# Kernel optimization log

Hardware: AMD Instinct MI355X
Metric: run time of the kernel (lower is better)

Reference implementation:

```python
import jax, jax.numpy as jnp
import numpy as np
from jax import lax

B, CIN, COUT, K, SDIM, H = 8, 512, 512, 3, 512, 32
EPS = 1e-8
LRELU_SLOPE = 0.2
ACT_SCALE = float(np.sqrt(2.0))


def setup_inputs() -> dict:
    key = jax.random.key(0)
    k1, k2, k3, k4 = jax.random.split(key, 4)
    return {
        "x": jax.random.normal(k1, (B, CIN, H, H), jnp.float32),
        "style": jax.random.normal(k2, (B, SDIM), jnp.float32),
        "weight": jax.random.normal(k3, (COUT, CIN, K, K), jnp.float32),
        "mod_w": jax.random.normal(k4, (CIN, SDIM), jnp.float32),
        "mod_b": jnp.ones((CIN,), jnp.float32),  # EqualLinear bias_init=1
        "bias": jnp.zeros((COUT,), jnp.float32),  # FusedLeakyReLU bias
    }


def _blur_kernel(c):
    bk = np.array([1.0, 3.0, 3.0, 1.0], np.float32)
    bk = bk[None, :] * bk[:, None]
    bk = bk / bk.sum() * 4.0  # upsample_factor ** 2
    return jnp.tile(jnp.asarray(bk)[None, None], (c, 1, 1, 1))  # (C,1,4,4)


def reference(x, style, weight, mod_w, mod_b, bias):
    b, cin, h, w = x.shape
    cout, k = weight.shape[0], weight.shape[-1]
    conv_scale = 1.0 / np.sqrt(cin * k * k)
    lin_scale = 1.0 / np.sqrt(mod_w.shape[1])

    # style modulation: EqualLinear(style_dim -> in_channel), bias_init=1
    s = style @ (mod_w * lin_scale).T + mod_b  # (B, Cin)

    # per-sample modulated weights (B, Cout, Cin, k, k)
    wmod = conv_scale * weight[None] * s[:, None, :, None, None]
    demod = lax.rsqrt(jnp.sum(wmod * wmod, axis=(2, 3, 4)) + EPS)
    wmod = wmod * demod[:, :, None, None, None]

    # conv_transpose2d(stride=2, pad=0) == conv with lhs_dilation=2, pad=k-1,
    # spatially-flipped kernel (torch transposes (Cout,Cin)->(Cin,Cout)).
    wflip = jnp.flip(wmod, (-2, -1))

    def convt(xi, wi):  # xi: (Cin,H,W), wi: (Cout,Cin,k,k)
        return lax.conv_general_dilated(
            xi[None], wi, (1, 1), [(k - 1, k - 1)] * 2,
            lhs_dilation=(2, 2),
            dimension_numbers=("NCHW", "OIHW", "NCHW"))[0]

    y = jax.vmap(convt)(x, wflip)  # (B, Cout, 2H+1, 2W+1)

    # Blur: upfirdn2d with pad=(1,1), depthwise 4x4 FIR (kernel symmetric)
    bk = _blur_kernel(cout)
    y = lax.conv_general_dilated(
        y, bk, (1, 1), [(1, 1), (1, 1)],
        feature_group_count=cout,
        dimension_numbers=("NCHW", "OIHW", "NCHW"))  # (B, Cout, 2H, 2W)

    # FusedLeakyReLU: leaky_relu(y + bias) * sqrt(2)
    z = y + bias[None, :, None, None]
    return jnp.where(z >= 0, z, LRELU_SLOPE * z) * ACT_SCALE
```

## Files before the change

### kernel.cpp

```cpp
#include <hip/hip_runtime.h>
#include <hip/hip_bf16.h>

#define NB 8
#define CIN 512
#define COUT 512
#define SDIM 512

typedef __attribute__((ext_vector_type(8))) short short8;
typedef __attribute__((ext_vector_type(4))) float f32x4;

static constexpr float CONV_SCALE = 0.014731391274719740f;
static constexpr float LIN_SCALE  = 0.044194173824159216f;

static constexpr size_t OFF_S     = 0;
static constexpr size_t OFF_WSQ   = 16384;
static constexpr size_t OFF_DEMOD = 1064960;
static constexpr size_t OFF_XP    = 1081344;
static constexpr size_t OFF_WP    = 10551296;
static constexpr size_t OFF_Y1    = 15269888;

static constexpr int NJOBS = 1060;

__device__ __forceinline__ int wpoff(int ps) {
  return ps == 0 ? 0 : ps == 1 ? 1048576 : ps == 2 ? 1572864 : 2097152;
}
__device__ __forceinline__ constexpr int PSPAD(int ps) {
  return ps == 0 ? 1090 : ps == 3 ? 1024 : 1056;
}
__device__ __forceinline__ constexpr int PLB(int ps) {
  return ps == 0 ? 0 : ps == 1 ? 4464640 : ps == 2 ? 8790016 : 13115392;
}

__device__ __forceinline__ short f2bf(float f) {
  unsigned u = __builtin_bit_cast(unsigned, f);
  unsigned r = (u + 0x7fffu + ((u >> 16) & 1u)) >> 16;
  return (short)r;
}
__device__ __forceinline__ float bf2f(unsigned short u) {
  return __builtin_bit_cast(float, (unsigned)u << 16);
}

__device__ __forceinline__ void load_lds16(const short* g, short* l) {
  __builtin_amdgcn_global_load_lds(
      (const __attribute__((address_space(1))) unsigned int*)g,
      (__attribute__((address_space(3))) unsigned int*)l, 16, 0, 0);
}

__global__ void k_prep1(const float* __restrict__ style, const float* __restrict__ mod_w,
                        const float* __restrict__ mod_b, float* __restrict__ s_out,
                        const float* __restrict__ w, short* __restrict__ wp,
                        float* __restrict__ wsq) {
  const int tid = threadIdx.x;
  if (blockIdx.x < 1024) {
    int idx = blockIdx.x * 256 + tid;
    int co = idx >> 9, ci = idx & 511;
    float wv[3][3];
    float sq = 0.f;
#pragma unroll
    for (int i = 0; i < 9; ++i) {
      float v = w[idx * 9 + i];
      wv[i / 3][i % 3] = v;
      sq += v * v;
    }
    wsq[idx] = sq * CONV_SCALE * CONV_SCALE;
#pragma unroll
    for (int wy = 0; wy < 3; ++wy)
#pragma unroll
      for (int wx = 0; wx < 3; ++wx) {
        int psy = (wy == 1) ? 1 : 0, psx = (wx == 1) ? 1 : 0;
        int u = psy ? 0 : (wy == 0 ? 1 : 0);
        int v = psx ? 0 : (wx == 0 ? 1 : 0);
        int ps = psy * 2 + psx;
        int tap = psy ? (psx ? 0 : v) : (psx ? u : u * 2 + v);
        int k = tap * 512 + ci;
        int elem = wpoff(ps) + ((k >> 6) * 512 + co) * 64 + (k & 63);
        wp[elem] = f2bf(wv[wy][wx] * CONV_SCALE);
      }
  } else {
    int wid = tid >> 6, lane = tid & 63;
    int ci = (blockIdx.x - 1024) * 4 + wid;
    float acc[NB] = {};
    for (int k = lane; k < SDIM; k += 64) {
      float wm = mod_w[ci * SDIM + k];
#pragma unroll
      for (int b = 0; b < NB; ++b) acc[b] += wm * style[b * SDIM + k];
    }
#pragma unroll
    for (int b = 0; b < NB; ++b) {
      float v = acc[b];
      for (int o = 32; o > 0; o >>= 1) v += __shfl_xor(v, o);
      if (lane == 0) s_out[b * CIN + ci] = v * LIN_SCALE + mod_b[ci];
    }
  }
}

__global__ void k_prep2(const float* __restrict__ wsq, const float* __restrict__ s,
                        float* __restrict__ demod,
                        const float* __restrict__ x, short* __restrict__ xp) {
  const int tid = threadIdx.x;
  if (blockIdx.x < 1024) {
    __shared__ float t[64][65];
    const int tx = tid & 63, ty = tid >> 6;
    int bx = blockIdx.x;
    int sp0 = (bx & 15) * 64, ci0 = ((bx >> 4) & 7) * 64, b = bx >> 7;
    for (int r = ty; r < 64; r += 4)
      t[r][tx] = x[(b * CIN + ci0 + r) * 1024 + sp0 + tx];
    __syncthreads();
    int ci = ci0 + tx;
    float sv = s[b * CIN + ci];
    for (int r = ty; r < 64; r += 4) {
      int sp = sp0 + r;
      int yy = sp >> 5, xx = sp & 31;
      xp[((b * 34 + yy + 1) * 34 + (xx + 1)) * 512 + ci] = f2bf(t[tx][r] * sv);
    }
  } else if (blockIdx.x < 1152) {
    int wid = tid >> 6, lane = tid & 63;
    int co = (blockIdx.x - 1024) * 4 + wid;
    float acc[NB] = {};
    for (int ci = lane; ci < CIN; ci += 64) {
      float wq = wsq[co * CIN + ci];
#pragma unroll
      for (int b = 0; b < NB; ++b) {
        float sv = s[b * CIN + ci];
        acc[b] += wq * sv * sv;
      }
    }
#pragma unroll
    for (int b = 0; b < NB; ++b) {
      float v = acc[b];
      for (int o = 32; o > 0; o >>= 1) v += __shfl_xor(v, o);
      if (lane == 0) demod[b * COUT + co] = rsqrtf(v + 1e-8f);
    }
  } else {
    int idx = blockIdx.x - 1152;
    int b = idx >> 2, part = idx & 3;
    unsigned* xpu = (unsigned*)xp;
    for (int k = 0; k < 33; ++k) {
      int c = part * 33 + k;
      int yy, xx;
      if (c < 34)       { yy = 0;            xx = c; }
      else if (c < 68)  { yy = 33;           xx = c - 34; }
      else if (c < 100) { yy = 1 + (c - 68); xx = 0; }
      else              { yy = 1 + (c - 100); xx = 33; }
      xpu[((((b * 34 + yy) * 34 + xx) * 512) >> 1) + tid] = 0u;
    }
  }
}

__global__ __launch_bounds__(256, 4) void k_gemm(const short* __restrict__ xp,
                                                 const short* __restrict__ wp,
                                                 short* __restrict__ y1) {
  __shared__ short sW[2][128 * 32];
  __shared__ short sX[2][128 * 32];

  const int tid = threadIdx.x;
  const int wid = tid >> 6, lane = tid & 63;
  const int hi = lane >> 4;
  const int wm = (wid >> 1) * 64, wn = (wid & 1) * 64;

  const int bx = blockIdx.x;
  const int xcd = bx & 7, ii = bx >> 3;
  const int j = (((ii >> 2) << 3) + xcd) * 4 + (ii & 3);
  if (j >= NJOBS) return;

  int ps, base;
  if (j < 276)      { ps = 0; base = 0; }
  else if (j < 540) { ps = 1; base = 276; }
  else if (j < 804) { ps = 2; base = 540; }
  else              { ps = 3; base = 804; }
  const int r = j - base;
  const int nb = r >> 2, mb = r & 3;
  const int psy = ps >> 1, psx = ps & 1;
  const int Ny = 33 - psy, Nx = 33 - psx;
  const int NyNx = Ny * Nx;
  const int N = NB * NyNx;
  const int n0 = nb * 128, m0 = mb * 128;
  const int KT32 = (2 - psy) * (2 - psx) * 16;
  const short* wpb = wp + wpoff(ps);

  int bb2[2], ay2[2], ax2[2];
#pragma unroll
  for (int i = 0; i < 2; ++i) {
    int n = n0 + i * 64 + (tid >> 2);
    if (n >= N) n = N - 1;
    int b = n / NyNx;
    int rem = n - b * NyNx;
    int a_y = rem / Nx;
    bb2[i] = b; ay2[i] = a_y; ax2[i] = rem - a_y * Nx;
  }

  auto STAGE = [&](int kt, int d) {
    int tap = kt >> 4, ci0 = (kt & 15) << 5;
    int oy, ox;
    if (ps == 0)      { oy = tap >> 1; ox = tap & 1; }
    else if (ps == 1) { oy = tap;      ox = 1; }
    else if (ps == 2) { oy = 1;        ox = tap; }
    else              { oy = 1;        ox = 1; }
#pragma unroll
    for (int i = 0; i < 2; ++i) {
      int seg = i * 256 + tid;
      int row = seg >> 2;
      int clog = (seg & 3) ^ ((row >> 1) & 3);
      const short* gw = wpb + ((kt >> 1) * 512 + m0 + row) * 64 + (kt & 1) * 32 + clog * 8;
      load_lds16(gw, &sW[d][seg * 8]);
    }
#pragma unroll
    for (int i = 0; i < 2; ++i) {
      int seg = i * 256 + tid;
      int row = seg >> 2;
      int clog = (seg & 3) ^ ((row >> 1) & 3);
      const short* gx = xp + ((bb2[i] * 34 + ay2[i] + oy) * 34 + ax2[i] + ox) * 512 + ci0 + clog * 8;
      load_lds16(gx, &sX[d][seg * 8]);
    }
  };

  int offA[4], offB[4];
#pragma unroll
  for (int f = 0; f < 4; ++f) {
    int ra = wm + f * 16 + (lane & 15);
    offA[f] = ra * 32 + ((hi ^ ((ra >> 1) & 3)) * 8);
    int rb = wn + f * 16 + (lane & 15);
    offB[f] = rb * 32 + ((hi ^ ((rb >> 1) & 3)) * 8);
  }

  f32x4 acc[4][4] = {};

  STAGE(0, 0);
  STAGE(1, 1);
  __syncthreads();

  for (int t = 0; t < KT32; ++t) {
    const short* W = sW[t & 1];
    const short* X = sX[t & 1];
    short8 af[4], bf[4];
#pragma unroll
    for (int f = 0; f < 4; ++f) af[f] = *(const short8*)&W[offA[f]];
#pragma unroll
    for (int f = 0; f < 4; ++f) bf[f] = *(const short8*)&X[offB[f]];

    __builtin_amdgcn_s_setprio(1);
#pragma unroll
    for (int mf = 0; mf < 4; ++mf)
#pragma unroll
      for (int nf = 0; nf < 4; ++nf)
        acc[mf][nf] = __builtin_amdgcn_mfma_f32_16x16x32_bf16(af[mf], bf[nf], acc[mf][nf], 0, 0, 0);
    __builtin_amdgcn_s_setprio(0);

    __syncthreads();
    if (t + 2 < KT32) STAGE(t + 2, t & 1);
  }

  const int psp = PSPAD(ps);
  const int plb = PLB(ps);
#pragma unroll
  for (int nf = 0; nf < 4; ++nf) {
    int n = n0 + wn + nf * 16 + (lane & 15);
    if (n < N) {
      int b = n / NyNx;
      int rem = n - b * NyNx;
      int nbase = plb + b * psp + rem;
#pragma unroll
      for (int mf = 0; mf < 4; ++mf) {
        int m = m0 + wm + mf * 16 + (lane >> 4) * 4;
#pragma unroll
        for (int rr = 0; rr < 4; ++rr)
          y1[nbase + (m + rr) * 8 * psp] = f2bf(acc[mf][nf][rr]);
      }
    }
  }
}

__global__ __launch_bounds__(256, 8) void k_blur(const short* __restrict__ y1,
                                                 const float* __restrict__ demod,
                                                 const float* __restrict__ bias,
                                                 float* __restrict__ out) {
  __shared__ float sin_[4][18 * 35];
  __shared__ float stmp[2][18][64];
  const int tid = threadIdx.x;
  const int bc = blockIdx.x & 4095;
  const int h = blockIdx.x >> 12;
  const int co = bc & 511, b = bc >> 9;
  const int m0v = h * 16;

  for (int i = tid; i < 4 * 18 * 35; i += 256) ((float*)sin_)[i] = 0.f;
  __syncthreads();

#pragma unroll
  for (int ps = 0; ps < 4; ++ps) {
    const int Nyv = 33 - (ps >> 1), Nxv = 33 - (ps & 1);
    const int total = Nyv * Nxv;
    const int estart = (h == 0) ? 0 : (m0v - 1) * Nxv;
    const int es = estart & ~1;
    const int eend = min(total, (m0v + 17) * Nxv);
    const short* pl = y1 + PLB(ps) + (co * NB + b) * PSPAD(ps);
    for (int e0 = es + tid * 2; e0 < eend; e0 += 512) {
      unsigned pair = *(const unsigned*)&pl[e0];
      int av0 = e0 / Nxv, ah0 = e0 - av0 * Nxv;
      int lr0 = av0 + 1 - m0v;
      if (lr0 >= 0 && lr0 < 18)
        sin_[ps][lr0 * 35 + ah0 + 1] = bf2f((unsigned short)(pair & 0xffffu));
      int e1 = e0 + 1;
      if (e1 < total) {
        int av1 = e1 / Nxv, ah1 = e1 - av1 * Nxv;
        int lr1 = av1 + 1 - m0v;
        if (lr1 >= 0 && lr1 < 18)
          sin_[ps][lr1 * 35 + ah1 + 1] = bf2f((unsigned short)(pair >> 16));
      }
    }
  }
  __syncthreads();

  const int q = tid & 63;
  const int mx = q >> 1, fx = q & 1;
  int xp0, xi0, xp1, xi1, xp2, xi2, xp3, xi3;
  if (fx) { xp0 = 0; xi0 = mx + 1; xp1 = 1; xi1 = mx + 1; xp2 = 0; xi2 = mx + 2; xp3 = 1; xi3 = mx + 2; }
  else    { xp0 = 1; xi0 = mx;     xp1 = 0; xi1 = mx + 1; xp2 = 1; xi2 = mx + 1; xp3 = 0; xi3 = mx + 2; }

  for (int rt = tid >> 6; rt < 36; rt += 4) {
    int pv = (rt >= 18) ? 1 : 0;
    int lr = rt - pv * 18;
    if (m0v + lr < 35) {
      float v = 0.25f * sin_[pv * 2 + xp0][lr * 35 + xi0]
              + 0.75f * sin_[pv * 2 + xp1][lr * 35 + xi1]
              + 0.75f * sin_[pv * 2 + xp2][lr * 35 + xi2]
              + 0.25f * sin_[pv * 2 + xp3][lr * 35 + xi3];
      stmp[pv][lr][q] = v;
    } else {
      stmp[pv][lr][q] = 0.f;
    }
  }
  __syncthreads();

  const float dm = demod[b * COUT + co], bs = bias[co];
  for (int pl_ = tid >> 6; pl_ < 32; pl_ += 4) {
    int myl = pl_ >> 1, fy = pl_ & 1;
    float v;
    if (fy) v = 0.25f * stmp[0][myl + 1][q] + 0.75f * stmp[1][myl + 1][q]
              + 0.75f * stmp[0][myl + 2][q] + 0.25f * stmp[1][myl + 2][q];
    else    v = 0.25f * stmp[1][myl][q]     + 0.75f * stmp[0][myl + 1][q]
              + 0.75f * stmp[1][myl + 1][q] + 0.25f * stmp[0][myl + 2][q];
    float val = dm * v + bs;
    int p = h * 32 + pl_;
    out[(bc * 64 + p) * 64 + q] = (val >= 0.f ? val : 0.2f * val) * 1.41421356237309515f;
  }
}

extern "C" void kernel_launch(void* const* d_in, const int* in_sizes, int n_in,
                              void* d_out, int out_size, void* d_ws, size_t ws_size,
                              hipStream_t stream) {
  const float* x      = (const float*)d_in[0];
  const float* style  = (const float*)d_in[1];
  const float* weight = (const float*)d_in[2];
  const float* mod_w  = (const float*)d_in[3];
  const float* mod_b  = (const float*)d_in[4];
  const float* bias   = (const float*)d_in[5];
  float* out = (float*)d_out;
  char* ws = (char*)d_ws;

  float* s     = (float*)(ws + OFF_S);
  float* wsq   = (float*)(ws + OFF_WSQ);
  float* demod = (float*)(ws + OFF_DEMOD);
  short* xp    = (short*)(ws + OFF_XP);
  short* wp    = (short*)(ws + OFF_WP);
  short* y1    = (short*)(ws + OFF_Y1);

  k_prep1<<<1152, 256, 0, stream>>>(style, mod_w, mod_b, s, weight, wp, wsq);
  k_prep2<<<1184, 256, 0, stream>>>(wsq, s, demod, x, xp);
  k_gemm<<<1088, 256, 0, stream>>>(xp, wp, y1);
  k_blur<<<8192, 256, 0, stream>>>(y1, demod, bias, out);
}
```

Baseline: 115.5 us.

## Enlarge GEMM block tile to 128x256 with each wave covering all M rows

The transposed-conv GEMM block tile grows from 128x128 to 128 (M) x 256 (N). Each of the four waves now computes a 128x64 slab instead of a 64x64 quadrant, and job counts and the grid are halved to match. Each X row's base pointer is precomputed and the swizzle offset hoisted out of the staging loop to cut address arithmetic. This roughly halves the number of times weight tiles are loaded per output and raises MFMA work per LDS read. In exchange it doubles accumulator registers and LDS per block, which lowers occupancy (launch bounds drop to 2 blocks per CU) and makes the last wave of blocks coarser.

```diff
diff --git a/kernel.cpp b/kernel.cpp
--- a/kernel.cpp
+++ b/kernel.cpp
@@ -19,7 +19,7 @@
 static constexpr size_t OFF_WP    = 10551296;
 static constexpr size_t OFF_Y1    = 15269888;
 
-static constexpr int NJOBS = 1060;
+static constexpr int NJOBS = 532;
 
 __device__ __forceinline__ int wpoff(int ps) {
   return ps == 0 ? 0 : ps == 1 ? 1048576 : ps == 2 ? 1572864 : 2097152;
@@ -147,16 +147,16 @@
   }
 }
 
-__global__ __launch_bounds__(256, 4) void k_gemm(const short* __restrict__ xp,
+__global__ __launch_bounds__(256, 2) void k_gemm(const short* __restrict__ xp,
                                                  const short* __restrict__ wp,
                                                  short* __restrict__ y1) {
-  __shared__ short sW[2][128 * 32];
-  __shared__ short sX[2][128 * 32];
+  __shared__ short sW[2][4096];
+  __shared__ short sX[2][8192];
 
   const int tid = threadIdx.x;
   const int wid = tid >> 6, lane = tid & 63;
   const int hi = lane >> 4;
-  const int wm = (wid >> 1) * 64, wn = (wid & 1) * 64;
+  const int wn = wid * 64;
 
   const int bx = blockIdx.x;
   const int xcd = bx & 7, ii = bx >> 3;
@@ -164,30 +164,32 @@
   if (j >= NJOBS) return;
 
   int ps, base;
-  if (j < 276)      { ps = 0; base = 0; }
-  else if (j < 540) { ps = 1; base = 276; }
-  else if (j < 804) { ps = 2; base = 540; }
-  else              { ps = 3; base = 804; }
+  if (j < 140)      { ps = 0; base = 0; }
+  else if (j < 272) { ps = 1; base = 140; }
+  else if (j < 404) { ps = 2; base = 272; }
+  else              { ps = 3; base = 404; }
   const int r = j - base;
   const int nb = r >> 2, mb = r & 3;
   const int psy = ps >> 1, psx = ps & 1;
   const int Ny = 33 - psy, Nx = 33 - psx;
   const int NyNx = Ny * Nx;
   const int N = NB * NyNx;
-  const int n0 = nb * 128, m0 = mb * 128;
+  const int n0 = nb * 256, m0 = mb * 128;
   const int KT32 = (2 - psy) * (2 - psx) * 16;
   const short* wpb = wp + wpoff(ps);
 
-  int bb2[2], ay2[2], ax2[2];
-#pragma unroll
-  for (int i = 0; i < 2; ++i) {
+  const short* xbase[4];
+#pragma unroll
+  for (int i = 0; i < 4; ++i) {
     int n = n0 + i * 64 + (tid >> 2);
     if (n >= N) n = N - 1;
     int b = n / NyNx;
     int rem = n - b * NyNx;
     int a_y = rem / Nx;
-    bb2[i] = b; ay2[i] = a_y; ax2[i] = rem - a_y * Nx;
-  }
+    int a_x = rem - a_y * Nx;
+    xbase[i] = xp + ((b * 34 + a_y) * 34 + a_x) * 512;
+  }
+  const int clog8 = (((tid & 3) ^ ((tid >> 3) & 3)) * 8);
 
   auto STAGE = [&](int kt, int d) {
     int tap = kt >> 4, ci0 = (kt & 15) << 5;
@@ -196,34 +198,33 @@
     else if (ps == 1) { oy = tap;      ox = 1; }
     else if (ps == 2) { oy = 1;        ox = tap; }
     else              { oy = 1;        ox = 1; }
+    const int goffX = (oy * 34 + ox) * 512 + ci0 + clog8;
 #pragma unroll
     for (int i = 0; i < 2; ++i) {
       int seg = i * 256 + tid;
-      int row = seg >> 2;
-      int clog = (seg & 3) ^ ((row >> 1) & 3);
-      const short* gw = wpb + ((kt >> 1) * 512 + m0 + row) * 64 + (kt & 1) * 32 + clog * 8;
+      const short* gw = wpb + ((kt >> 1) * 512 + m0 + (seg >> 2)) * 64 + (kt & 1) * 32 + clog8;
       load_lds16(gw, &sW[d][seg * 8]);
     }
 #pragma unroll
-    for (int i = 0; i < 2; ++i) {
+    for (int i = 0; i < 4; ++i) {
       int seg = i * 256 + tid;
-      int row = seg >> 2;
-      int clog = (seg & 3) ^ ((row >> 1) & 3);
-      const short* gx = xp + ((bb2[i] * 34 + ay2[i] + oy) * 34 + ax2[i] + ox) * 512 + ci0 + clog * 8;
-      load_lds16(gx, &sX[d][seg * 8]);
+      load_lds16(xbase[i] + goffX, &sX[d][seg * 8]);
     }
   };
 
-  int offA[4], offB[4];
+  int offA[8], offB[4];
+#pragma unroll
+  for (int f = 0; f < 8; ++f) {
+    int ra = f * 16 + (lane & 15);
+    offA[f] = ra * 32 + ((hi ^ ((ra >> 1) & 3)) * 8);
+  }
 #pragma unroll
   for (int f = 0; f < 4; ++f) {
-    int ra = wm + f * 16 + (lane & 15);
-    offA[f] = ra * 32 + ((hi ^ ((ra >> 1) & 3)) * 8);
     int rb = wn + f * 16 + (lane & 15);
     offB[f] = rb * 32 + ((hi ^ ((rb >> 1) & 3)) * 8);
   }
 
-  f32x4 acc[4][4] = {};
+  f32x4 acc[8][4] = {};
 
   STAGE(0, 0);
   STAGE(1, 1);
@@ -232,18 +233,18 @@
   for (int t = 0; t < KT32; ++t) {
     const short* W = sW[t & 1];
     const short* X = sX[t & 1];
-    short8 af[4], bf[4];
-#pragma unroll
-    for (int f = 0; f < 4; ++f) af[f] = *(const short8*)&W[offA[f]];
+    short8 bf[4];
 #pragma unroll
     for (int f = 0; f < 4; ++f) bf[f] = *(const short8*)&X[offB[f]];
 
     __builtin_amdgcn_s_setprio(1);
 #pragma unroll
-    for (int mf = 0; mf < 4; ++mf)
+    for (int mf = 0; mf < 8; ++mf) {
+      short8 af = *(const short8*)&W[offA[mf]];
 #pragma unroll
       for (int nf = 0; nf < 4; ++nf)
-        acc[mf][nf] = __builtin_amdgcn_mfma_f32_16x16x32_bf16(af[mf], bf[nf], acc[mf][nf], 0, 0, 0);
+        acc[mf][nf] = __builtin_amdgcn_mfma_f32_16x16x32_bf16(af, bf[nf], acc[mf][nf], 0, 0, 0);
+    }
     __builtin_amdgcn_s_setprio(0);
 
     __syncthreads();
@@ -260,8 +261,8 @@
       int rem = n - b * NyNx;
       int nbase = plb + b * psp + rem;
 #pragma unroll
-      for (int mf = 0; mf < 4; ++mf) {
-        int m = m0 + wm + mf * 16 + (lane >> 4) * 4;
+      for (int mf = 0; mf < 8; ++mf) {
+        int m = m0 + mf * 16 + (lane >> 4) * 4;
 #pragma unroll
         for (int rr = 0; rr < 4; ++rr)
           y1[nbase + (m + rr) * 8 * psp] = f2bf(acc[mf][nf][rr]);
@@ -366,6 +367,6 @@
 
   k_prep1<<<1152, 256, 0, stream>>>(style, mod_w, mod_b, s, weight, wp, wsq);
   k_prep2<<<1184, 256, 0, stream>>>(wsq, s, demod, x, xp);
-  k_gemm<<<1088, 256, 0, stream>>>(xp, wp, y1);
+  k_gemm<<<544, 256, 0, stream>>>(xp, wp, y1);
   k_blur<<<8192, 256, 0, stream>>>(y1, demod, bias, out);
 }
```

Measured after the change: 124.0 us. 7.4% more time.
